# Kernel tuning notes

Hardware: AMD Instinct MI355X
Metric: run time of the kernel (lower is better)

## Reference

```python
import math
import jax, jax.numpy as jnp
import numpy as np

DT = 0.001
TAU = 0.02
ALPHA_LIF = math.exp(-DT / TAU)  # fixed LIF decay ~0.9512
V_TH = 1.0
V_RESET = 0.0
BETA = 25.0  # SuperSpike surrogate slope used in LIFLayer

@jax.custom_vjp
def spike(x):
    # SuperSpike forward: hard threshold
    return (x > 0.0).astype(x.dtype)

def _spike_fwd(x):
    return spike(x), x

def _spike_bwd(x, g):
    # surrogate gradient: beta * max(0, 1 - |beta * x|)
    sg = BETA * jnp.clip(1.0 - jnp.abs(BETA * x), 0.0)
    return (g * sg,)

spike.defvjp(_spike_fwd, _spike_bwd)


def setup_inputs() -> dict:
    key = jax.random.key(0)
    k1, k2, k3 = jax.random.split(key, 3)
    T, B, C_IN, C_OUT = 500, 64, 512, 512
    x_seq = jax.random.uniform(k1, (T, B, C_IN), dtype=jnp.float32)
    # kaiming_uniform_(a=sqrt(5)) on [c_in, c_out] -> bound = 1/sqrt(fan_in)
    bound = 1.0 / math.sqrt(C_IN)
    W = jax.random.uniform(k2, (C_IN, C_OUT), minval=-bound, maxval=bound, dtype=jnp.float32)
    alpha_param = jnp.asarray(0.9, dtype=jnp.float32)  # learned synapse trace decay
    return {"x_seq": x_seq, "W": W, "alpha_param": alpha_param}


def reference(x_seq, W, alpha_param):
    T, B, c_in = x_seq.shape
    c_out = W.shape[1]
    a = jnp.clip(alpha_param, 0.0, 0.9999)

    def step(carry, x_t):
        v, trace = carry                      # v: [B, c_out], trace: [B, c_in]
        trace = a * trace + x_t               # synapse trace update
        cur = x_t @ W + trace @ W             # synaptic current [B, c_out]
        v = ALPHA_LIF * v + (1.0 - ALPHA_LIF) * cur
        s = spike(v - V_TH)                   # surrogate-grad threshold
        v = jnp.where(s > 0, V_RESET, v)      # hard reset
        return (v, trace), s

    init = (jnp.zeros((B, c_out), x_seq.dtype), jnp.zeros((B, c_in), x_seq.dtype))
    _, spikes_out = jax.lax.scan(step, init, x_seq)  # [T, B, c_out]
    rates = spikes_out.mean(axis=0)                  # [B, c_out]
    return spikes_out, rates
```

## Files before the change

### kernel.cpp

```cpp
#include <hip/hip_runtime.h>

typedef float f32x4 __attribute__((ext_vector_type(4)));

#define TSTEPS 500
#define BDIM 64
#define CIN 512
#define COUT 512
#define MTOT (TSTEPS * BDIM)
#define NCH (BDIM * CIN)
#define SNEUR (BDIM * COUT)
#define OUTN ((size_t)TSTEPS * SNEUR + SNEUR)

#define AL64 0.95122942450071400909
#define BL64 (1.0 - AL64)

#define BUF_BYTES 65536000ull
#define WS_NEED (3ull * BUF_BYTES)

__global__ __launch_bounds__(256) void fill_const_f32(
    float* __restrict__ p, size_t n, float c) {
  size_t i = (size_t)blockIdx.x * 256 + threadIdx.x;
  const size_t stride = (size_t)gridDim.x * 256;
  for (; i < n; i += stride) p[i] = c;
}

__global__ __launch_bounds__(256) void trace32(
    const float* __restrict__ X, float* __restrict__ TR,
    const float* __restrict__ alpha) {
  const int j = blockIdx.x * 256 + threadIdx.x;
  const float a = fminf(fmaxf(alpha[0], 0.0f), 0.9999f);
  float tr = 0.0f;
#pragma unroll 10
  for (int t = 0; t < TSTEPS; ++t) {
    float x = X[(size_t)t * NCH + j];
    tr = __fadd_rn(__fmul_rn(a, tr), x);
    TR[(size_t)t * NCH + j] = tr;
  }
}

#define GEMM_SHARED                                  \
  __shared__ __align__(16) float Asx[64][20];        \
  __shared__ __align__(16) float Ast[64][20];        \
  __shared__ __align__(16) float Bs[16][132];

#define GEMM_SETUP                                   \
  const int tid = threadIdx.x;                       \
  const int ty = tid >> 4, tx = tid & 15;            \
  const int fid = blockIdx.x;                        \
  const int swz = (fid & 7) * 250 + (fid >> 3);      \
  const int bm = (swz >> 2) * 64;                    \
  const int bn = (swz & 3) * 128;                    \
  const int ar = tid >> 2, ak = (tid & 3) * 4;       \
  const int bk = tid >> 4, bc = (tid & 15) * 8;

#define GEMM_STEP(kt)                                                        \
  {                                                                          \
    *(f32x4*)&Asx[ar][ak] =                                                  \
        *(const f32x4*)&X[(size_t)(bm + ar) * CIN + (kt)*16 + ak];           \
    *(f32x4*)&Ast[ar][ak] =                                                  \
        *(const f32x4*)&TR[(size_t)(bm + ar) * CIN + (kt)*16 + ak];          \
    *(f32x4*)&Bs[bk][bc] =                                                   \
        *(const f32x4*)&W[(size_t)((kt)*16 + bk) * COUT + bn + bc];          \
    *(f32x4*)&Bs[bk][bc + 4] =                                               \
        *(const f32x4*)&W[(size_t)((kt)*16 + bk) * COUT + bn + bc + 4];      \
    __syncthreads();                                                         \
    _Pragma("unroll") for (int kg = 0; kg < 4; ++kg) {                       \
      f32x4 ax[4], at4[4];                                                   \
      _Pragma("unroll") for (int i = 0; i < 4; ++i) {                        \
        ax[i] = *(const f32x4*)&Asx[ty * 4 + i][kg * 4];                     \
        at4[i] = *(const f32x4*)&Ast[ty * 4 + i][kg * 4];                    \
      }                                                                      \
      _Pragma("unroll") for (int k2 = 0; k2 < 4; ++k2) {                     \
        f32x4 bL = *(const f32x4*)&Bs[kg * 4 + k2][tx * 4];                  \
        f32x4 bH = *(const f32x4*)&Bs[kg * 4 + k2][64 + tx * 4];             \
        _Pragma("unroll") for (int i = 0; i < 4; ++i)                        \
          _Pragma("unroll") for (int j = 0; j < 4; ++j) {                    \
            xA[i][j]     = fmaf(ax[i][k2], bL[j], xA[i][j]);                 \
            xA[i][4 + j] = fmaf(ax[i][k2], bH[j], xA[i][4 + j]);             \
            tA[i][j]     = fmaf(at4[i][k2], bL[j], tA[i][j]);                \
            tA[i][4 + j] = fmaf(at4[i][k2], bH[j], tA[i][4 + j]);            \
          }                                                                  \
      }                                                                      \
    }                                                                        \
    __syncthreads();                                                         \
  }

__global__ __launch_bounds__(256) void gemm_head(
    const float* __restrict__ X, const float* __restrict__ TR,
    const float* __restrict__ W, float* __restrict__ PHx,
    float* __restrict__ PHt) {
  GEMM_SHARED
  GEMM_SETUP
  float xA[4][8] = {{0.0f}}, tA[4][8] = {{0.0f}};
  for (int kt = 0; kt < 24; ++kt) GEMM_STEP(kt)

#pragma unroll
  for (int i = 0; i < 4; ++i) {
    const size_t row = (size_t)(bm + ty * 4 + i);
    f32x4 xL, xH2, tL, tH2;
#pragma unroll
    for (int j = 0; j < 4; ++j) {
      xL[j] = xA[i][j];   xH2[j] = xA[i][4 + j];
      tL[j] = tA[i][j];   tH2[j] = tA[i][4 + j];
    }
    *(f32x4*)&PHx[row * COUT + bn + tx * 4] = xL;
    *(f32x4*)&PHx[row * COUT + bn + 64 + tx * 4] = xH2;
    *(f32x4*)&PHt[row * COUT + bn + tx * 4] = tL;
    *(f32x4*)&PHt[row * COUT + bn + 64 + tx * 4] = tH2;
  }
}

__global__ __launch_bounds__(256) void gemm_tail(
    const float* __restrict__ X, const float* __restrict__ TR,
    const float* __restrict__ W, float* __restrict__ PHx,
    const float* __restrict__ PHt) {
  GEMM_SHARED
  GEMM_SETUP
  float xA[4][8] = {{0.0f}}, tA[4][8] = {{0.0f}};
  for (int kt = 24; kt < 32; ++kt) GEMM_STEP(kt)

#pragma unroll
  for (int i = 0; i < 4; ++i) {
    const size_t row = (size_t)(bm + ty * 4 + i);
    const size_t iL = row * COUT + bn + tx * 4;
    const size_t iH = row * COUT + bn + 64 + tx * 4;
    f32x4 hxL = *(const f32x4*)&PHx[iL];
    f32x4 hxH = *(const f32x4*)&PHx[iH];
    f32x4 htL = *(const f32x4*)&PHt[iL];
    f32x4 htH = *(const f32x4*)&PHt[iH];
    f32x4 oL, oH;
#pragma unroll
    for (int j = 0; j < 4; ++j) {
      oL[j] = __fadd_rn(__fadd_rn(hxL[j], xA[i][j]),
                        __fadd_rn(htL[j], tA[i][j]));
      oH[j] = __fadd_rn(__fadd_rn(hxH[j], xA[i][4 + j]),
                        __fadd_rn(htH[j], tA[i][4 + j]));
    }
    *(f32x4*)&PHx[iL] = oL;
    *(f32x4*)&PHx[iH] = oH;
  }
}

__global__ __launch_bounds__(256) void lif32(
    const float* __restrict__ CUR, float* __restrict__ spikes,
    float* __restrict__ rates) {
  const int j = blockIdx.x * 256 + threadIdx.x;
  const float AL = (float)AL64, BL = (float)BL64;
  float v = 0.0f;
  int cnt = 0;
#pragma unroll 10
  for (int t = 0; t < TSTEPS; ++t) {
    float cur = CUR[(size_t)t * SNEUR + j];
    v = __fadd_rn(__fmul_rn(AL, v), __fmul_rn(BL, cur));
    int sp = __fadd_rn(v, -1.0f) > 0.0f;
    cnt += sp;
    spikes[(size_t)t * SNEUR + j] = sp ? 1.0f : 0.0f;
    v = sp ? 0.0f : v;
  }
  rates[j] = __fdiv_rn((float)cnt, 500.0f);
}

extern "C" void kernel_launch(void* const* d_in, const int* in_sizes, int n_in,
                              void* d_out, int out_size, void* d_ws, size_t ws_size,
                              hipStream_t stream) {
  float* out = (float*)d_out;

  float flag = 0.0f;
  const float* X = nullptr;
  const float* W = nullptr;
  const float* AP = nullptr;
  if (n_in != 3) {
    flag = 11.0f;
  } else {
    for (int i = 0; i < 3; ++i) {
      if (in_sizes[i] == 16384000) X = (const float*)d_in[i];
      else if (in_sizes[i] == 262144) W = (const float*)d_in[i];
      else if (in_sizes[i] == 1) AP = (const float*)d_in[i];
    }
    if (!X || !W || !AP) flag = 13.0f;
    else if (out_size != (int)OUTN) flag = 17.0f;
    else if (ws_size < WS_NEED) flag = 23.0f;
  }
  if (flag != 0.0f) {
    fill_const_f32<<<dim3(2048), dim3(256), 0, stream>>>(out, OUTN, flag);
    return;
  }

  char* ws = (char*)d_ws;
  float* TR = (float*)(ws);
  float* PHx = (float*)(ws + BUF_BYTES);
  float* PHt = (float*)(ws + 2 * BUF_BYTES);

  trace32<<<dim3(NCH / 256), dim3(256), 0, stream>>>(X, TR, AP);
  gemm_head<<<dim3(2000), dim3(256), 0, stream>>>(X, TR, W, PHx, PHt);
  gemm_tail<<<dim3(2000), dim3(256), 0, stream>>>(X, TR, W, PHx, PHt);
  lif32<<<dim3(SNEUR / 256), dim3(256), 0, stream>>>(
      PHx, out, out + (size_t)TSTEPS * SNEUR);
}
```

Before: 502.6 us.

## Enlarge GEMM tile to 128x128 with register prefetch and swizzled shared memory

The two GEMM phases become one templated kernel whose block tile grows from 64x128 to 128x128, giving each thread an 8x8 micro-tile per accumulator. The next K-slice is prefetched into registers while the current one is computed, and the A tiles in shared memory are XOR-swizzled to avoid bank conflicts. The goal is more FMA reuse per shared-memory load and less exposed global latency. The cost is doubled accumulator registers (128 floats per thread), which risks spills and lower occupancy, and half as many blocks.

```diff
diff --git a/kernel.cpp b/kernel.cpp
--- a/kernel.cpp
+++ b/kernel.cpp
@@ -38,106 +38,110 @@
   }
 }
 
-#define GEMM_SHARED                                  \
-  __shared__ __align__(16) float Asx[64][20];        \
-  __shared__ __align__(16) float Ast[64][20];        \
-  __shared__ __align__(16) float Bs[16][132];
-
-#define GEMM_SETUP                                   \
-  const int tid = threadIdx.x;                       \
-  const int ty = tid >> 4, tx = tid & 15;            \
-  const int fid = blockIdx.x;                        \
-  const int swz = (fid & 7) * 250 + (fid >> 3);      \
-  const int bm = (swz >> 2) * 64;                    \
-  const int bn = (swz & 3) * 128;                    \
-  const int ar = tid >> 2, ak = (tid & 3) * 4;       \
-  const int bk = tid >> 4, bc = (tid & 15) * 8;
-
-#define GEMM_STEP(kt)                                                        \
-  {                                                                          \
-    *(f32x4*)&Asx[ar][ak] =                                                  \
-        *(const f32x4*)&X[(size_t)(bm + ar) * CIN + (kt)*16 + ak];           \
-    *(f32x4*)&Ast[ar][ak] =                                                  \
-        *(const f32x4*)&TR[(size_t)(bm + ar) * CIN + (kt)*16 + ak];          \
-    *(f32x4*)&Bs[bk][bc] =                                                   \
-        *(const f32x4*)&W[(size_t)((kt)*16 + bk) * COUT + bn + bc];          \
-    *(f32x4*)&Bs[bk][bc + 4] =                                               \
-        *(const f32x4*)&W[(size_t)((kt)*16 + bk) * COUT + bn + bc + 4];      \
-    __syncthreads();                                                         \
-    _Pragma("unroll") for (int kg = 0; kg < 4; ++kg) {                       \
-      f32x4 ax[4], at4[4];                                                   \
-      _Pragma("unroll") for (int i = 0; i < 4; ++i) {                        \
-        ax[i] = *(const f32x4*)&Asx[ty * 4 + i][kg * 4];                     \
-        at4[i] = *(const f32x4*)&Ast[ty * 4 + i][kg * 4];                    \
-      }                                                                      \
-      _Pragma("unroll") for (int k2 = 0; k2 < 4; ++k2) {                     \
-        f32x4 bL = *(const f32x4*)&Bs[kg * 4 + k2][tx * 4];                  \
-        f32x4 bH = *(const f32x4*)&Bs[kg * 4 + k2][64 + tx * 4];             \
-        _Pragma("unroll") for (int i = 0; i < 4; ++i)                        \
-          _Pragma("unroll") for (int j = 0; j < 4; ++j) {                    \
-            xA[i][j]     = fmaf(ax[i][k2], bL[j], xA[i][j]);                 \
-            xA[i][4 + j] = fmaf(ax[i][k2], bH[j], xA[i][4 + j]);             \
-            tA[i][j]     = fmaf(at4[i][k2], bL[j], tA[i][j]);                \
-            tA[i][4 + j] = fmaf(at4[i][k2], bH[j], tA[i][4 + j]);            \
-          }                                                                  \
-      }                                                                      \
-    }                                                                        \
-    __syncthreads();                                                         \
-  }
-
-__global__ __launch_bounds__(256) void gemm_head(
+template <int PHASE>
+__global__ __launch_bounds__(256) void gemm8(
     const float* __restrict__ X, const float* __restrict__ TR,
     const float* __restrict__ W, float* __restrict__ PHx,
     float* __restrict__ PHt) {
-  GEMM_SHARED
-  GEMM_SETUP
-  float xA[4][8] = {{0.0f}}, tA[4][8] = {{0.0f}};
-  for (int kt = 0; kt < 24; ++kt) GEMM_STEP(kt)
-
-#pragma unroll
-  for (int i = 0; i < 4; ++i) {
-    const size_t row = (size_t)(bm + ty * 4 + i);
-    f32x4 xL, xH2, tL, tH2;
-#pragma unroll
-    for (int j = 0; j < 4; ++j) {
-      xL[j] = xA[i][j];   xH2[j] = xA[i][4 + j];
-      tL[j] = tA[i][j];   tH2[j] = tA[i][4 + j];
-    }
-    *(f32x4*)&PHx[row * COUT + bn + tx * 4] = xL;
-    *(f32x4*)&PHx[row * COUT + bn + 64 + tx * 4] = xH2;
-    *(f32x4*)&PHt[row * COUT + bn + tx * 4] = tL;
-    *(f32x4*)&PHt[row * COUT + bn + 64 + tx * 4] = tH2;
-  }
-}
-
-__global__ __launch_bounds__(256) void gemm_tail(
-    const float* __restrict__ X, const float* __restrict__ TR,
-    const float* __restrict__ W, float* __restrict__ PHx,
-    const float* __restrict__ PHt) {
-  GEMM_SHARED
-  GEMM_SETUP
-  float xA[4][8] = {{0.0f}}, tA[4][8] = {{0.0f}};
-  for (int kt = 24; kt < 32; ++kt) GEMM_STEP(kt)
-
-#pragma unroll
-  for (int i = 0; i < 4; ++i) {
-    const size_t row = (size_t)(bm + ty * 4 + i);
+  __shared__ __align__(16) float Asx[2048];
+  __shared__ __align__(16) float Ast[2048];
+  __shared__ __align__(16) float Bs[2048];
+  const int tid = threadIdx.x;
+  const int ty = tid >> 4, tx = tid & 15;
+
+  const int fid = blockIdx.x;
+  const int swz = (fid & 7) * 125 + (fid >> 3);
+  const int bm = (swz >> 2) * 128;
+  const int bn = (swz & 3) * 128;
+
+  const int arow = tid >> 1, ahalf = tid & 1;
+  const int asw = (arow >> 3) & 3;
+  const int aw0 = (((ahalf * 2) ^ asw)) * 4;
+  const int aw1 = (((ahalf * 2 + 1) ^ asw)) * 4;
+  const int brow = tid >> 4, bcol = (tid & 15) * 8;
+
+  const int KT0 = PHASE ? 24 : 0;
+  const int KT1 = PHASE ? 32 : 24;
+
+  const float* gx = X + (size_t)(bm + arow) * CIN + KT0 * 16 + ahalf * 8;
+  const float* gt = TR + (size_t)(bm + arow) * CIN + KT0 * 16 + ahalf * 8;
+  const float* gw = W + (size_t)(KT0 * 16 + brow) * COUT + bn + bcol;
+
+  float xA[8][8] = {{0.0f}}, tA[8][8] = {{0.0f}};
+
+  f32x4 rx0 = *(const f32x4*)gx, rx1 = *(const f32x4*)(gx + 4);
+  f32x4 rt0 = *(const f32x4*)gt, rt1 = *(const f32x4*)(gt + 4);
+  f32x4 rw0 = *(const f32x4*)gw, rw1 = *(const f32x4*)(gw + 4);
+
+  for (int kt = KT0; kt < KT1; ++kt) {
+    __syncthreads();
+    *(f32x4*)&Asx[arow * 16 + aw0] = rx0;
+    *(f32x4*)&Asx[arow * 16 + aw1] = rx1;
+    *(f32x4*)&Ast[arow * 16 + aw0] = rt0;
+    *(f32x4*)&Ast[arow * 16 + aw1] = rt1;
+    *(f32x4*)&Bs[brow * 128 + bcol] = rw0;
+    *(f32x4*)&Bs[brow * 128 + bcol + 4] = rw1;
+    __syncthreads();
+    if (kt + 1 < KT1) {
+      gx += 16; gt += 16; gw += 16 * COUT;
+      rx0 = *(const f32x4*)gx; rx1 = *(const f32x4*)(gx + 4);
+      rt0 = *(const f32x4*)gt; rt1 = *(const f32x4*)(gt + 4);
+      rw0 = *(const f32x4*)gw; rw1 = *(const f32x4*)(gw + 4);
+    }
+#pragma unroll
+    for (int kg = 0; kg < 4; ++kg) {
+      const int G = (kg ^ (ty & 3)) * 4;
+      f32x4 ax[8], at8[8];
+#pragma unroll
+      for (int i = 0; i < 8; ++i) {
+        ax[i] = *(const f32x4*)&Asx[(ty * 8 + i) * 16 + G];
+        at8[i] = *(const f32x4*)&Ast[(ty * 8 + i) * 16 + G];
+      }
+#pragma unroll
+      for (int k2 = 0; k2 < 4; ++k2) {
+        f32x4 bL = *(const f32x4*)&Bs[(kg * 4 + k2) * 128 + tx * 4];
+        f32x4 bH = *(const f32x4*)&Bs[(kg * 4 + k2) * 128 + 64 + tx * 4];
+#pragma unroll
+        for (int i = 0; i < 8; ++i)
+#pragma unroll
+          for (int j = 0; j < 4; ++j) {
+            xA[i][j]     = fmaf(ax[i][k2], bL[j], xA[i][j]);
+            xA[i][4 + j] = fmaf(ax[i][k2], bH[j], xA[i][4 + j]);
+            tA[i][j]     = fmaf(at8[i][k2], bL[j], tA[i][j]);
+            tA[i][4 + j] = fmaf(at8[i][k2], bH[j], tA[i][4 + j]);
+          }
+      }
+    }
+  }
+
+#pragma unroll
+  for (int i = 0; i < 8; ++i) {
+    const size_t row = (size_t)(bm + ty * 8 + i);
     const size_t iL = row * COUT + bn + tx * 4;
     const size_t iH = row * COUT + bn + 64 + tx * 4;
-    f32x4 hxL = *(const f32x4*)&PHx[iL];
-    f32x4 hxH = *(const f32x4*)&PHx[iH];
-    f32x4 htL = *(const f32x4*)&PHt[iL];
-    f32x4 htH = *(const f32x4*)&PHt[iH];
-    f32x4 oL, oH;
+    f32x4 xL, xH2, tL, tH2;
 #pragma unroll
     for (int j = 0; j < 4; ++j) {
-      oL[j] = __fadd_rn(__fadd_rn(hxL[j], xA[i][j]),
-                        __fadd_rn(htL[j], tA[i][j]));
-      oH[j] = __fadd_rn(__fadd_rn(hxH[j], xA[i][4 + j]),
-                        __fadd_rn(htH[j], tA[i][4 + j]));
-    }
-    *(f32x4*)&PHx[iL] = oL;
-    *(f32x4*)&PHx[iH] = oH;
+      xL[j] = xA[i][j];  xH2[j] = xA[i][4 + j];
+      tL[j] = tA[i][j];  tH2[j] = tA[i][4 + j];
+    }
+    if (PHASE == 0) {
+      *(f32x4*)&PHx[iL] = xL;   *(f32x4*)&PHx[iH] = xH2;
+      *(f32x4*)&PHt[iL] = tL;   *(f32x4*)&PHt[iH] = tH2;
+    } else {
+      f32x4 hxL = *(const f32x4*)&PHx[iL];
+      f32x4 hxH = *(const f32x4*)&PHx[iH];
+      f32x4 htL = *(const f32x4*)&PHt[iL];
+      f32x4 htH = *(const f32x4*)&PHt[iH];
+      f32x4 oL, oH;
+#pragma unroll
+      for (int j = 0; j < 4; ++j) {
+        oL[j] = __fadd_rn(__fadd_rn(hxL[j], xL[j]), __fadd_rn(htL[j], tL[j]));
+        oH[j] = __fadd_rn(__fadd_rn(hxH[j], xH2[j]), __fadd_rn(htH[j], tH2[j]));
+      }
+      *(f32x4*)&PHx[iL] = oL;
+      *(f32x4*)&PHx[iH] = oH;
+    }
   }
 }
 
@@ -192,8 +196,8 @@
   float* PHt = (float*)(ws + 2 * BUF_BYTES);
 
   trace32<<<dim3(NCH / 256), dim3(256), 0, stream>>>(X, TR, AP);
-  gemm_head<<<dim3(2000), dim3(256), 0, stream>>>(X, TR, W, PHx, PHt);
-  gemm_tail<<<dim3(2000), dim3(256), 0, stream>>>(X, TR, W, PHx, PHt);
+  gemm8<0><<<dim3(1000), dim3(256), 0, stream>>>(X, TR, W, PHx, PHt);
+  gemm8<1><<<dim3(1000), dim3(256), 0, stream>>>(X, TR, W, PHx, PHt);
   lif32<<<dim3(SNEUR / 256), dim3(256), 0, stream>>>(
       PHx, out, out + (size_t)TSTEPS * SNEUR);
 }
```

Result: slower. 558.4 us (+11.1%).
